# Kernel optimization log

Measured on AMD Instinct MI355X. Metric: run time of the kernel, lower is better.

The kernel has to match this reference:

```python
import jax, jax.numpy as jnp
import numpy as np

CHUNK = 128


def selective_scan(x, A, Bm, Cm, dt, chunk_size):
    # x: [B,L,H,hd], Bm/Cm: [B,L,H,ds], A/dt: [H]. L must be divisible by chunk_size.
    Bb, L, H, hd = x.shape
    ds = Bm.shape[-1]
    cs = chunk_size
    nc = L // cs
    decay = jnp.exp(A * dt)  # [H]
    x_c = x.reshape(Bb, nc, cs, H, hd).transpose(0, 1, 3, 2, 4)   # [B,nc,H,cs,hd]
    B_c = Bm.reshape(Bb, nc, cs, H, ds).transpose(0, 1, 3, 2, 4)  # [B,nc,H,cs,ds]
    C_c = Cm.reshape(Bb, nc, cs, H, ds).transpose(0, 1, 3, 2, 4)
    x_dt = x_c * dt[None, None, :, None, None]
    idx = jnp.arange(cs, dtype=x.dtype)
    diff = idx[:, None] - idx[None, :]
    # causal intra-chunk decay matrix [H,cs,cs]
    L_mat = jnp.where(diff >= 0, decay[:, None, None] ** jnp.maximum(diff, 0.0), 0.0)
    CB = jnp.einsum('bnhid,bnhjd->bnhij', C_c, B_c)          # [B,nc,H,cs,cs]
    y_diag = jnp.einsum('bnhij,bnhjd->bnhid', CB * L_mat[None, None], x_dt)
    rev = jnp.arange(cs - 1, -1, -1, dtype=x.dtype)
    decay_rev = decay[:, None] ** rev[None, :]               # [H,cs]
    B_w = B_c * decay_rev[None, None, :, :, None]
    states = jnp.einsum('bnhjs,bnhjd->bnhsd', B_w, x_dt)     # [B,nc,H,ds,hd]
    cidx = jnp.arange(nc, dtype=x.dtype)
    shift = cidx[:, None] - cidx[None, :] - 1.0
    chunk_decay = decay ** cs
    M = jnp.where(shift >= 0, chunk_decay[:, None, None] ** jnp.maximum(shift, 0.0), 0.0)  # [H,nc,nc]
    h_carry = jnp.einsum('hij,bjhsd->bihsd', M, states)      # [B,nc,H,ds,hd]
    decay_out = decay[:, None] ** (idx[None, :] + 1.0)       # [H,cs]
    y_off = jnp.einsum('bnhis,bnhsd->bnhid', C_c, h_carry) * decay_out[None, None, :, :, None]
    y = (y_diag + y_off).transpose(0, 1, 3, 2, 4).reshape(Bb, L, H, hd)
    return y


def setup_inputs() -> dict:
    key = jax.random.key(0)
    ks = jax.random.split(key, 9)
    B, L, d_model, d_inner, H, ds, K = 2, 4096, 1024, 2048, 16, 128, 4
    s_dm = 1.0 / np.sqrt(d_model)
    s_di = 1.0 / np.sqrt(d_inner)
    x = jax.random.normal(ks[0], (B, L, d_model), jnp.float32)
    x_prenorm = jax.random.normal(ks[1], (B, L, d_model), jnp.float32)
    in_proj_w = jax.random.normal(ks[2], (2 * d_inner, d_model), jnp.float32) * s_dm
    conv_w = jax.random.normal(ks[3], (d_inner, 1, K), jnp.float32) * 0.5
    conv_b = jax.random.normal(ks[4], (d_inner,), jnp.float32) * 0.01
    B_proj_w = jax.random.normal(ks[5], (H * ds, d_model), jnp.float32) * s_dm
    C_proj_w = jax.random.normal(ks[6], (H * ds, d_model), jnp.float32) * s_dm
    dt_init = jax.random.uniform(ks[7], (H,), jnp.float32, 0.001, 0.1)
    dt_bias = dt_init + jnp.log(-jnp.expm1(-dt_init))  # inverse softplus
    A_log = jnp.log(jnp.arange(1, H + 1, dtype=jnp.float32))
    D_param = jnp.ones((H,), jnp.float32)
    out_proj_w = jax.random.normal(ks[8], (d_model, d_inner), jnp.float32) * s_di
    return dict(x=x, x_prenorm=x_prenorm, in_proj_w=in_proj_w, conv_w=conv_w,
                conv_b=conv_b, B_proj_w=B_proj_w, C_proj_w=C_proj_w,
                dt_bias=dt_bias, A_log=A_log, D_param=D_param, out_proj_w=out_proj_w)


def reference(x, x_prenorm, in_proj_w, conv_w, conv_b, B_proj_w, C_proj_w,
              dt_bias, A_log, D_param, out_proj_w):
    Bb, L, d_model = x.shape
    H = A_log.shape[0]
    ds = B_proj_w.shape[0] // H
    vg = x @ in_proj_w.T                        # [B,L,2*d_inner]
    d_inner = vg.shape[-1] // 2
    value, gate = vg[..., :d_inner], vg[..., d_inner:]
    K = conv_w.shape[-1]
    # causal depthwise conv1d (torch pads K-1 both sides then truncates right)
    v = jax.lax.conv_general_dilated(
        value.transpose(0, 2, 1), conv_w, (1,), [(K - 1, 0)],
        feature_group_count=d_inner, dimension_numbers=('NCH', 'OIH', 'NCH'))
    v = v + conv_b[None, :, None]
    value = jax.nn.silu(v.transpose(0, 2, 1))   # [B,L,d_inner]
    Bm = (x_prenorm @ B_proj_w.T).reshape(Bb, L, H, ds)
    Cm = (x_prenorm @ C_proj_w.T).reshape(Bb, L, H, ds)
    dt = jax.nn.softplus(dt_bias)
    A = -jnp.exp(A_log)
    hd = d_inner // H
    vh = value.reshape(Bb, L, H, hd)
    y = selective_scan(vh, A, Bm, Cm, dt, CHUNK)
    y = y + D_param[None, None, :, None] * vh
    y = y.reshape(Bb, L, d_inner) * jax.nn.silu(gate)
    return y @ out_proj_w.T
```

## Files before the change

kernel.cpp:

```cpp
#include <hip/hip_runtime.h>
#include <hip/hip_bf16.h>

#define NB 2
#define LSEQ 4096
#define DM 1024
#define DI 2048
#define NH 16
#define DSZ 128
#define CS 128
#define NCHUNK 32

using bf16 = __hip_bfloat16;
typedef __attribute__((ext_vector_type(8))) short short8;
typedef __attribute__((ext_vector_type(4))) float f32x4;

__device__ __forceinline__ float b2f(unsigned short u) {
    union { unsigned i; float f; } c; c.i = ((unsigned)u) << 16; return c.f;
}
__device__ __forceinline__ bf16 f2bf(float v) { return __float2bfloat16(v); }
__device__ __forceinline__ float bf2f(bf16 v) { return __bfloat162float(v); }

__device__ __forceinline__ float head_dt(const float* dt_bias, int h) {
    return log1pf(expf(dt_bias[h]));
}
__device__ __forceinline__ float head_l2dec(const float* dt_bias, const float* A_log, int h, float* dt_out) {
    float dt = head_dt(dt_bias, h);
    *dt_out = dt;
    return -expf(A_log[h]) * dt * 1.4426950408889634f;
}

__device__ __forceinline__ void storeC(bf16* C, size_t idx, float v) { C[idx] = f2bf(v); }
__device__ __forceinline__ void storeC(float* C, size_t idx, float v) { C[idx] = v; }

__device__ __forceinline__ void gload16(const bf16* g, bf16* l) {
    __builtin_amdgcn_global_load_lds(
        (const __attribute__((address_space(1))) void*)g,
        (__attribute__((address_space(3))) void*)l, 16, 0, 0);
}

__global__ __launch_bounds__(256) void cast_f2b(const float* __restrict__ in,
                                                bf16* __restrict__ out, long n) {
    long i = ((long)blockIdx.x * 256 + threadIdx.x) * 8;
    if (i >= n) return;
    float4 a = *reinterpret_cast<const float4*>(in + i);
    float4 b = *reinterpret_cast<const float4*>(in + i + 4);
    union { bf16 h[8]; short8 v; } o;
    o.h[0] = f2bf(a.x); o.h[1] = f2bf(a.y); o.h[2] = f2bf(a.z); o.h[3] = f2bf(a.w);
    o.h[4] = f2bf(b.x); o.h[5] = f2bf(b.y); o.h[6] = f2bf(b.z); o.h[7] = f2bf(b.w);
    *reinterpret_cast<short8*>(out + i) = o.v;
}

template <int MODE, typename TO>
__global__ __launch_bounds__(256) void gemm_mfma(const bf16* __restrict__ A,
                                                 const bf16* __restrict__ W,
                                                 TO* __restrict__ C0, TO* __restrict__ C1,
                                                 int N, int K) {
    __shared__ bf16 As[2][128 * 32];
    __shared__ bf16 Ws[2][128 * 32];
    const int tid = threadIdx.x;
    const int lane = tid & 63, w = tid >> 6;
    const int wr = w >> 1, wc = w & 1;
    const int bm = blockIdx.y * 128, bn = blockIdx.x * 128;
    const int srow = lane >> 2;
    const int skoff = (((lane & 3) ^ ((lane >> 2) & 3)) * 8);
    const int g0 = w * 2, g1 = w * 2 + 1;
    const int fr = lane & 15;
    const int fk = (((lane >> 4) ^ (lane & 3)) * 8);
    f32x4 acc[4][4] = {};
#define STAGE(buf, kt)                                                                  \
    do {                                                                                \
        gload16(A + (size_t)(bm + g0 * 16 + srow) * K + (kt) + skoff, &As[buf][g0 * 512]); \
        gload16(A + (size_t)(bm + g1 * 16 + srow) * K + (kt) + skoff, &As[buf][g1 * 512]); \
        gload16(W + (size_t)(bn + g0 * 16 + srow) * K + (kt) + skoff, &Ws[buf][g0 * 512]); \
        gload16(W + (size_t)(bn + g1 * 16 + srow) * K + (kt) + skoff, &Ws[buf][g1 * 512]); \
    } while (0)
    STAGE(0, 0);
    __syncthreads();
    const int NT = K / 32;
    int cur = 0;
    for (int t = 0; t < NT; ++t) {
        if (t + 1 < NT) STAGE(cur ^ 1, (t + 1) * 32);
        short8 af[4], bfr[4];
#pragma unroll
        for (int mi = 0; mi < 4; ++mi)
            af[mi] = *reinterpret_cast<const short8*>(&As[cur][(wr * 64 + mi * 16 + fr) * 32 + fk]);
#pragma unroll
        for (int ni = 0; ni < 4; ++ni)
            bfr[ni] = *reinterpret_cast<const short8*>(&Ws[cur][(wc * 64 + ni * 16 + fr) * 32 + fk]);
#pragma unroll
        for (int mi = 0; mi < 4; ++mi)
#pragma unroll
            for (int ni = 0; ni < 4; ++ni)
                acc[mi][ni] = __builtin_amdgcn_mfma_f32_16x16x32_bf16(af[mi], bfr[ni], acc[mi][ni], 0, 0, 0);
        __syncthreads();
        cur ^= 1;
    }
#undef STAGE
    const int orow0 = (lane >> 4) * 4;
    const int ocol = lane & 15;
#pragma unroll
    for (int mi = 0; mi < 4; ++mi)
#pragma unroll
        for (int ni = 0; ni < 4; ++ni) {
            int col = bn + wc * 64 + ni * 16 + ocol;
#pragma unroll
            for (int r = 0; r < 4; ++r) {
                int row = bm + wr * 64 + mi * 16 + orow0 + r;
                float v = acc[mi][ni][r];
                if (MODE == 1) {
                    if (col < DI) storeC(C0, (size_t)row * DI + col, v);
                    else          storeC(C1, (size_t)row * DI + (col - DI), v);
                } else {
                    storeC(C0, (size_t)row * N + col, v);
                }
            }
        }
}

__global__ __launch_bounds__(256) void conv_xdt(const bf16* __restrict__ vpre,
                                                const float* __restrict__ cw,
                                                const float* __restrict__ cb,
                                                const float* __restrict__ dt_bias,
                                                bf16* __restrict__ XDT) {
    __shared__ bf16 Ts[131][136];
    __shared__ bf16 T2[128][136];
    __shared__ float wks[128][4];
    __shared__ float cbs[128];
    const int tid = threadIdx.x;
    const int bid = blockIdx.x;
    const int h = bid & 15, g = bid >> 4;
    const int n31 = g & 31;
    const float dt = head_dt(dt_bias, h);
    if (tid < 128) {
        float4 w4 = *reinterpret_cast<const float4*>(cw + (h * 128 + tid) * 4);
        wks[tid][0] = w4.x; wks[tid][1] = w4.y; wks[tid][2] = w4.z; wks[tid][3] = w4.w;
        cbs[tid] = cb[h * 128 + tid];
    }
    {
        const int lr = tid >> 4, c8 = (tid & 15) * 8;
        for (int i0 = 0; i0 < 144; i0 += 16) {
            int i = i0 + lr;
            if (i < 131) {
                short8 v = {0, 0, 0, 0, 0, 0, 0, 0};
                if (!(n31 == 0 && i < 3))
                    v = *reinterpret_cast<const short8*>(vpre + (size_t)(g * 128 - 3 + i) * 2048 + h * 128 + c8);
                *reinterpret_cast<short8*>(&Ts[i][c8]) = v;
            }
        }
    }
    __syncthreads();
    {
        const int jr = tid >> 4, d8 = (tid & 15) * 8;
        for (int j0 = 0; j0 < 128; j0 += 16) {
            int j = j0 + jr;
            union { bf16 hh[8]; short8 v; } o;
#pragma unroll
            for (int e = 0; e < 8; ++e) {
                int d = d8 + e;
                float s = cbs[d];
#pragma unroll
                for (int k = 0; k < 4; ++k) s += wks[d][k] * bf2f(Ts[j + k][d]);
                float sil = s / (1.f + expf(-s));
                o.hh[e] = f2bf(sil * dt);
            }
            *reinterpret_cast<short8*>(&T2[j][d8]) = o.v;
        }
    }
    __syncthreads();
    {
        const size_t ob = (size_t)bid * 16384;
        const int d = tid & 127;
        for (int jg = (tid >> 7); jg < 16; jg += 2) {
            int j0 = jg * 8;
            union { bf16 hh[8]; short8 v; } o;
#pragma unroll
            for (int e = 0; e < 8; ++e) o.hh[e] = T2[j0 + e][d];
            *reinterpret_cast<short8*>(XDT + ob + (size_t)d * 128 + j0) = o.v;
        }
    }
}

__global__ __launch_bounds__(256) void transpose_bt(const bf16* __restrict__ in, bf16* __restrict__ outp,
                                                    const float* __restrict__ dt_bias,
                                                    const float* __restrict__ A_log) {
    __shared__ bf16 Ts[128][136];
    __shared__ float dpow[128];
    const int tid = threadIdx.x;
    const int bid = blockIdx.x;
    const int h = bid & 15, bn = bid >> 4;
    float dt; float l2d = head_l2dec(dt_bias, A_log, h, &dt);
    if (tid < 128) dpow[tid] = exp2f((float)(127 - tid) * l2d);
    const size_t base = (size_t)bn * CS * 2048 + (size_t)h * 128;
    {
        const int jr = tid >> 4, c8 = (tid & 15) * 8;
        for (int j0 = 0; j0 < 128; j0 += 16)
            *reinterpret_cast<short8*>(&Ts[j0 + jr][c8]) =
                *reinterpret_cast<const short8*>(in + base + (size_t)(j0 + jr) * 2048 + c8);
    }
    __syncthreads();
    const size_t ob = (size_t)bid * 16384;
    const int d = tid & 127;
    for (int jg = (tid >> 7); jg < 16; jg += 2) {
        int j0 = jg * 8;
        union { bf16 h8[8]; short8 v; } o;
#pragma unroll
        for (int e = 0; e < 8; ++e) o.h8[e] = f2bf(bf2f(Ts[j0 + e][d]) * dpow[j0 + e]);
        *reinterpret_cast<short8*>(outp + ob + (size_t)d * 128 + j0) = o.v;
    }
}

__global__ __launch_bounds__(256) void chunk_statesT(const bf16* __restrict__ XDT,
                                                     const bf16* BTg,
                                                     bf16* STT) {
    __shared__ bf16 XTs[128][72];
    __shared__ bf16 BTs[128][72];
    const int tid = threadIdx.x;
    const size_t ob = (size_t)blockIdx.x * 16384;
    const int lane = tid & 63, w = tid >> 6;
    const int fr = lane & 15, fk = (lane >> 4) * 8;
    f32x4 acc[2][8] = {};
    for (int j0 = 0; j0 < 128; j0 += 64) {
        for (int rr = 0; rr < 128; rr += 32) {
            int row = rr + (tid >> 3);
            int col = (tid & 7) * 8;
            *reinterpret_cast<short8*>(&XTs[row][col]) =
                *reinterpret_cast<const short8*>(XDT + ob + (size_t)row * 128 + j0 + col);
            *reinterpret_cast<short8*>(&BTs[row][col]) =
                *reinterpret_cast<const short8*>(BTg + ob + (size_t)row * 128 + j0 + col);
        }
        __syncthreads();
        __builtin_amdgcn_s_setprio(1);
#pragma unroll
        for (int ks = 0; ks < 2; ++ks) {
            short8 a[2], bfr[8];
#pragma unroll
            for (int mi = 0; mi < 2; ++mi)
                a[mi] = *reinterpret_cast<const short8*>(&XTs[w * 32 + mi * 16 + fr][ks * 32 + fk]);
#pragma unroll
            for (int ni = 0; ni < 8; ++ni)
                bfr[ni] = *reinterpret_cast<const short8*>(&BTs[ni * 16 + fr][ks * 32 + fk]);
#pragma unroll
            for (int mi = 0; mi < 2; ++mi)
#pragma unroll
                for (int ni = 0; ni < 8; ++ni)
                    acc[mi][ni] = __builtin_amdgcn_mfma_f32_16x16x32_bf16(a[mi], bfr[ni], acc[mi][ni], 0, 0, 0);
        }
        __builtin_amdgcn_s_setprio(0);
        __syncthreads();
    }
    const int orow0 = (lane >> 4) * 4, ocol = lane & 15;
#pragma unroll
    for (int mi = 0; mi < 2; ++mi)
#pragma unroll
        for (int ni = 0; ni < 8; ++ni) {
            int s = ni * 16 + ocol;
#pragma unroll
            for (int r = 0; r < 4; ++r) {
                int d = w * 32 + mi * 16 + orow0 + r;
                STT[ob + (size_t)d * 128 + s] = f2bf(acc[mi][ni][r]);
            }
        }
}

__global__ __launch_bounds__(256) void scan_kernel(bf16* __restrict__ ST,
                                                   const float* __restrict__ dt_bias,
                                                   const float* __restrict__ A_log) {
    const int q = blockIdx.x & 7;
    const int h = (blockIdx.x >> 3) & 15;
    const int b = blockIdx.x >> 7;
    float dt; float l2d = head_l2dec(dt_bias, A_log, h, &dt);
    float cd = exp2f(128.f * l2d);
    const int tid = threadIdx.x;
    float r[8] = {};
    for (int n = 0; n < NCHUNK; ++n) {
        size_t base = ((size_t)((b * NCHUNK + n) * NH + h)) * 16384 + (size_t)q * 2048;
#pragma unroll
        for (int e = 0; e < 8; ++e) {
            size_t idx = base + e * 256 + tid;
            float v = bf2f(ST[idx]);
            ST[idx] = f2bf(r[e]);
            r[e] = cd * r[e] + v;
        }
    }
}

__global__ __launch_bounds__(256) void chunk_cbl_y(const bf16* __restrict__ Bm, const bf16* __restrict__ Cm,
                                                   const bf16* __restrict__ STT, const bf16* __restrict__ XDT,
                                                   const float* __restrict__ dt_bias,
                                                   const float* __restrict__ A_log,
                                                   const float* __restrict__ D_param,
                                                   bf16* __restrict__ gateY) {
    __shared__ char smem[53248];
    bf16 (*T1)[72]  = reinterpret_cast<bf16(*)[72]>(smem);
    bf16 (*Ps)[136] = reinterpret_cast<bf16(*)[136]>(smem + 18432);
    bf16 (*Bst)[72] = reinterpret_cast<bf16(*)[72]>(smem + 18432);
    const int tid = threadIdx.x;
    const int bid = blockIdx.x;
    const int h = bid & 15, g = bid >> 4;
    float dt; float l2d = head_l2dec(dt_bias, A_log, h, &dt);
    const size_t base = (size_t)g * CS * 2048 + (size_t)h * 128;
    const size_t ob = (size_t)bid * 16384;
    const int lane = tid & 63, w = tid >> 6;
    const int fr = lane & 15, fk = (lane >> 4) * 8;
    const int orow0 = (lane >> 4) * 4, ocol = lane & 15;
    const int strow = tid >> 3, stcol = (tid & 7) * 8;
    f32x4 pacc[2][8] = {};
    for (int s0 = 0; s0 < 128; s0 += 64) {
        for (int rr = 0; rr < 128; rr += 32) {
            int row = rr + strow;
            *reinterpret_cast<short8*>(&T1[row][stcol]) =
                *reinterpret_cast<const short8*>(Cm + base + (size_t)row * 2048 + s0 + stcol);
            *reinterpret_cast<short8*>(&Bst[row][stcol]) =
                *reinterpret_cast<const short8*>(Bm + base + (size_t)row * 2048 + s0 + stcol);
        }
        __syncthreads();
        __builtin_amdgcn_s_setprio(1);
#pragma unroll
        for (int ks = 0; ks < 2; ++ks) {
            short8 a[2], bfr[8];
#pragma unroll
            for (int mi = 0; mi < 2; ++mi)
                a[mi] = *reinterpret_cast<const short8*>(&T1[w * 32 + mi * 16 + fr][ks * 32 + fk]);
#pragma unroll
            for (int ni = 0; ni < 8; ++ni)
                bfr[ni] = *reinterpret_cast<const short8*>(&Bst[ni * 16 + fr][ks * 32 + fk]);
#pragma unroll
            for (int mi = 0; mi < 2; ++mi)
#pragma unroll
                for (int ni = 0; ni < 8; ++ni)
                    pacc[mi][ni] = __builtin_amdgcn_mfma_f32_16x16x32_bf16(a[mi], bfr[ni], pacc[mi][ni], 0, 0, 0);
        }
        __builtin_amdgcn_s_setprio(0);
        __syncthreads();
    }
#pragma unroll
    for (int mi = 0; mi < 2; ++mi)
#pragma unroll
        for (int ni = 0; ni < 8; ++ni) {
            int j = ni * 16 + ocol;
#pragma unroll
            for (int r = 0; r < 4; ++r) {
                int i = w * 32 + mi * 16 + orow0 + r;
                float v = (i >= j) ? pacc[mi][ni][r] * exp2f((float)(i - j) * l2d) : 0.f;
                Ps[i][j] = f2bf(v);
            }
        }
    f32x4 acc[2][8] = {};
    for (int hk = 0; hk < 2; ++hk) {
        for (int rr = 0; rr < 128; rr += 32) {
            int row = rr + strow;
            *reinterpret_cast<short8*>(&T1[row][stcol]) =
                *reinterpret_cast<const short8*>(STT + ob + (size_t)row * 128 + hk * 64 + stcol);
        }
        __syncthreads();
        __builtin_amdgcn_s_setprio(1);
#pragma unroll
        for (int ks = 0; ks < 2; ++ks) {
            short8 a[2], bfr[8];
#pragma unroll
            for (int mi = 0; mi < 2; ++mi)
                a[mi] = *reinterpret_cast<const short8*>(Cm + base + (size_t)(w * 32 + mi * 16 + fr) * 2048 + hk * 64 + ks * 32 + fk);
#pragma unroll
            for (int ni = 0; ni < 8; ++ni)
                bfr[ni] = *reinterpret_cast<const short8*>(&T1[ni * 16 + fr][ks * 32 + fk]);
#pragma unroll
            for (int mi = 0; mi < 2; ++mi)
#pragma unroll
                for (int ni = 0; ni < 8; ++ni)
                    acc[mi][ni] = __builtin_amdgcn_mfma_f32_16x16x32_bf16(a[mi], bfr[ni], acc[mi][ni], 0, 0, 0);
        }
        __builtin_amdgcn_s_setprio(0);
        __syncthreads();
    }
#pragma unroll
    for (int mi = 0; mi < 2; ++mi)
#pragma unroll
        for (int r = 0; r < 4; ++r) {
            int i = w * 32 + mi * 16 + orow0 + r;
            float sc = exp2f((float)(i + 1) * l2d);
#pragma unroll
            for (int ni = 0; ni < 8; ++ni) acc[mi][ni][r] *= sc;
        }
    for (int j0 = 0; j0 < 128; j0 += 64) {
        for (int rr = 0; rr < 128; rr += 32) {
            int row = rr + strow;
            *reinterpret_cast<short8*>(&T1[row][stcol]) =
                *reinterpret_cast<const short8*>(XDT + ob + (size_t)row * 128 + j0 + stcol);
        }
        __syncthreads();
        __builtin_amdgcn_s_setprio(1);
#pragma unroll
        for (int ks = 0; ks < 2; ++ks) {
            short8 a[2], bfr[8];
#pragma unroll
            for (int mi = 0; mi < 2; ++mi)
                a[mi] = *reinterpret_cast<const short8*>(&Ps[w * 32 + mi * 16 + fr][j0 + ks * 32 + fk]);
#pragma unroll
            for (int ni = 0; ni < 8; ++ni)
                bfr[ni] = *reinterpret_cast<const short8*>(&T1[ni * 16 + fr][ks * 32 + fk]);
#pragma unroll
            for (int mi = 0; mi < 2; ++mi)
#pragma unroll
                for (int ni = 0; ni < 8; ++ni)
                    acc[mi][ni] = __builtin_amdgcn_mfma_f32_16x16x32_bf16(a[mi], bfr[ni], acc[mi][ni], 0, 0, 0);
        }
        __builtin_amdgcn_s_setprio(0);
        __syncthreads();
    }
    const float Dv = D_param[h];
    const float inv_dt = 1.f / dt;
#pragma unroll
    for (int mi = 0; mi < 2; ++mi)
#pragma unroll
        for (int ni = 0; ni < 8; ++ni) {
            int d = ni * 16 + ocol;
#pragma unroll
            for (int r = 0; r < 4; ++r) {
                int i = w * 32 + mi * 16 + orow0 + r;
                size_t idx = base + (size_t)i * 2048 + d;
                float v = bf2f(XDT[ob + (size_t)d * 128 + i]) * inv_dt;
                float yv = acc[mi][ni][r] + Dv * v;
                float gq = bf2f(gateY[idx]);
                gateY[idx] = f2bf(yv * gq / (1.f + expf(-gq)));
            }
        }
}

extern "C" void kernel_launch(void* const* d_in, const int* in_sizes, int n_in,
                              void* d_out, int out_size, void* d_ws, size_t ws_size,
                              hipStream_t stream) {
    (void)out_size;
    static const int exp_sizes[11] = {
        NB * LSEQ * DM, NB * LSEQ * DM, 2 * DI * DM, DI * 4, DI,
        NH * DSZ * DM, NH * DSZ * DM, NH, NH, NH, DM * DI
    };
    if (n_in != 11) return;
    for (int i = 0; i < 11; ++i) if (in_sizes[i] != exp_sizes[i]) return;

    const float* x         = (const float*)d_in[0];
    const float* x_prenorm = (const float*)d_in[1];
    const float* in_proj_w = (const float*)d_in[2];
    const float* conv_w    = (const float*)d_in[3];
    const float* conv_b    = (const float*)d_in[4];
    const float* B_proj_w  = (const float*)d_in[5];
    const float* C_proj_w  = (const float*)d_in[6];
    const float* dt_bias   = (const float*)d_in[7];
    const float* A_log     = (const float*)d_in[8];
    const float* D_param   = (const float*)d_in[9];
    const float* out_proj_w= (const float*)d_in[10];
    float* out = (float*)d_out;

    const size_t NE = (size_t)NB * LSEQ * DI;
    const size_t SLOT = NE * 2;
    if (ws_size < 5 * SLOT) return;
    char* ws = (char*)d_ws;
    bf16* S0 = (bf16*)(ws);
    bf16* S1 = (bf16*)(ws + SLOT);
    bf16* S2 = (bf16*)(ws + 2 * SLOT);
    bf16* S3 = (bf16*)(ws + 3 * SLOT);
    bf16* S4 = (bf16*)(ws + 4 * SLOT);

    bf16* xb   = (bf16*)d_out;
    bf16* wBCb = (bf16*)((char*)d_out + 16777216);

    const int M = NB * LSEQ;
    const int NC = NB * NCHUNK * NH;
    dim3 blk(256);

    cast_f2b<<<dim3(4096), blk, 0, stream>>>(x, xb, (long)NB * LSEQ * DM);
    cast_f2b<<<dim3(2048), blk, 0, stream>>>(in_proj_w, S3, (long)2 * DI * DM);
    gemm_mfma<1, bf16><<<dim3(2 * DI / 128, M / 128), blk, 0, stream>>>(xb, S3, S0, S1, 2 * DI, DM);
    conv_xdt<<<dim3(NC), blk, 0, stream>>>(S0, conv_w, conv_b, dt_bias, S2);
    cast_f2b<<<dim3(4096), blk, 0, stream>>>(x_prenorm, xb, (long)NB * LSEQ * DM);
    cast_f2b<<<dim3(1024), blk, 0, stream>>>(B_proj_w, wBCb, (long)NH * DSZ * DM);
    cast_f2b<<<dim3(1024), blk, 0, stream>>>(C_proj_w, wBCb + (size_t)NH * DSZ * DM, (long)NH * DSZ * DM);
    gemm_mfma<1, bf16><<<dim3(2 * DI / 128, M / 128), blk, 0, stream>>>(xb, wBCb, S3, S4, 2 * DI, DM);
    transpose_bt<<<dim3(NC), blk, 0, stream>>>(S3, S0, dt_bias, A_log);
    chunk_statesT<<<dim3(NC), blk, 0, stream>>>(S2, S0, S0);
    scan_kernel<<<dim3(NB * NH * 8), blk, 0, stream>>>(S0, dt_bias, A_log);
    chunk_cbl_y<<<dim3(NC), blk, 0, stream>>>(S3, S4, S0, S2, dt_bias, A_log, D_param, S1);
    cast_f2b<<<dim3(1024), blk, 0, stream>>>(out_proj_w, S3, (long)DM * DI);
    gemm_mfma<2, float><<<dim3(DM / 128, M / 128), blk, 0, stream>>>(S1, S3, out, nullptr, DM, DI);
}
```

Baseline: 385.7 us.

## Fuse B transpose and decay scaling into BC projection GEMM epilogue; merge casts

The B/C projection GEMM gains a mode that, for B-column tiles, stages the tile transposed in shared memory, applies the per-position decay powers and writes the decay-weighted transposed B layout directly. This removes the separate transpose_bt kernel, which re-read B from global memory. The three fp32-to-bf16 casts for x_prenorm and the B/C weights are also merged into one launch. In exchange the GEMM's shared memory grows to hold the transpose buffer and half of its blocks run an extra epilogue.

```diff
diff --git a/kernel.cpp b/kernel.cpp
--- a/kernel.cpp
+++ b/kernel.cpp
@@ -50,13 +50,35 @@
     *reinterpret_cast<short8*>(out + i) = o.v;
 }
 
+__global__ __launch_bounds__(256) void cast3_f2b(const float* __restrict__ a, bf16* __restrict__ da, long na,
+                                                 const float* __restrict__ b, bf16* __restrict__ db, long nb,
+                                                 const float* __restrict__ c, bf16* __restrict__ dc, long nc) {
+    long i = ((long)blockIdx.x * 256 + threadIdx.x) * 8;
+    const float* src; bf16* dst; long off;
+    if (i < na)            { src = a; dst = da; off = i; }
+    else if (i < na + nb)  { src = b; dst = db; off = i - na; }
+    else if (i < na + nb + nc) { src = c; dst = dc; off = i - na - nb; }
+    else return;
+    float4 x = *reinterpret_cast<const float4*>(src + off);
+    float4 y = *reinterpret_cast<const float4*>(src + off + 4);
+    union { bf16 h[8]; short8 v; } o;
+    o.h[0] = f2bf(x.x); o.h[1] = f2bf(x.y); o.h[2] = f2bf(x.z); o.h[3] = f2bf(x.w);
+    o.h[4] = f2bf(y.x); o.h[5] = f2bf(y.y); o.h[6] = f2bf(y.z); o.h[7] = f2bf(y.w);
+    *reinterpret_cast<short8*>(dst + off) = o.v;
+}
+
 template <int MODE, typename TO>
 __global__ __launch_bounds__(256) void gemm_mfma(const bf16* __restrict__ A,
                                                  const bf16* __restrict__ W,
                                                  TO* __restrict__ C0, TO* __restrict__ C1,
+                                                 bf16* __restrict__ C2,
+                                                 const float* dt_bias, const float* A_log,
                                                  int N, int K) {
-    __shared__ bf16 As[2][128 * 32];
-    __shared__ bf16 Ws[2][128 * 32];
+    __shared__ char smem[35328];
+    bf16* Asb = reinterpret_cast<bf16*>(smem);
+    bf16* Wsb = reinterpret_cast<bf16*>(smem + 16384);
+    bf16 (*TP)[136] = reinterpret_cast<bf16(*)[136]>(smem);
+    float* dpw = reinterpret_cast<float*>(smem + 34816);
     const int tid = threadIdx.x;
     const int lane = tid & 63, w = tid >> 6;
     const int wr = w >> 1, wc = w & 1;
@@ -66,13 +88,18 @@
     const int g0 = w * 2, g1 = w * 2 + 1;
     const int fr = lane & 15;
     const int fk = (((lane >> 4) ^ (lane & 3)) * 8);
+    if (MODE == 3 && bn < DI && tid < 128) {
+        float dtq;
+        float l2d = head_l2dec(dt_bias, A_log, blockIdx.x & 15, &dtq);
+        dpw[tid] = exp2f((float)(127 - tid) * l2d);
+    }
     f32x4 acc[4][4] = {};
-#define STAGE(buf, kt)                                                                  \
-    do {                                                                                \
-        gload16(A + (size_t)(bm + g0 * 16 + srow) * K + (kt) + skoff, &As[buf][g0 * 512]); \
-        gload16(A + (size_t)(bm + g1 * 16 + srow) * K + (kt) + skoff, &As[buf][g1 * 512]); \
-        gload16(W + (size_t)(bn + g0 * 16 + srow) * K + (kt) + skoff, &Ws[buf][g0 * 512]); \
-        gload16(W + (size_t)(bn + g1 * 16 + srow) * K + (kt) + skoff, &Ws[buf][g1 * 512]); \
+#define STAGE(buf, kt)                                                                        \
+    do {                                                                                      \
+        gload16(A + (size_t)(bm + g0 * 16 + srow) * K + (kt) + skoff, Asb + (buf) * 4096 + g0 * 512); \
+        gload16(A + (size_t)(bm + g1 * 16 + srow) * K + (kt) + skoff, Asb + (buf) * 4096 + g1 * 512); \
+        gload16(W + (size_t)(bn + g0 * 16 + srow) * K + (kt) + skoff, Wsb + (buf) * 4096 + g0 * 512); \
+        gload16(W + (size_t)(bn + g1 * 16 + srow) * K + (kt) + skoff, Wsb + (buf) * 4096 + g1 * 512); \
     } while (0)
     STAGE(0, 0);
     __syncthreads();
@@ -83,10 +110,10 @@
         short8 af[4], bfr[4];
 #pragma unroll
         for (int mi = 0; mi < 4; ++mi)
-            af[mi] = *reinterpret_cast<const short8*>(&As[cur][(wr * 64 + mi * 16 + fr) * 32 + fk]);
+            af[mi] = *reinterpret_cast<const short8*>(Asb + cur * 4096 + (wr * 64 + mi * 16 + fr) * 32 + fk);
 #pragma unroll
         for (int ni = 0; ni < 4; ++ni)
-            bfr[ni] = *reinterpret_cast<const short8*>(&Ws[cur][(wc * 64 + ni * 16 + fr) * 32 + fk]);
+            bfr[ni] = *reinterpret_cast<const short8*>(Wsb + cur * 4096 + (wc * 64 + ni * 16 + fr) * 32 + fk);
 #pragma unroll
         for (int mi = 0; mi < 4; ++mi)
 #pragma unroll
@@ -107,7 +134,7 @@
             for (int r = 0; r < 4; ++r) {
                 int row = bm + wr * 64 + mi * 16 + orow0 + r;
                 float v = acc[mi][ni][r];
-                if (MODE == 1) {
+                if (MODE == 1 || MODE == 3) {
                     if (col < DI) storeC(C0, (size_t)row * DI + col, v);
                     else          storeC(C1, (size_t)row * DI + (col - DI), v);
                 } else {
@@ -115,6 +142,33 @@
                 }
             }
         }
+    if (MODE == 3 && bn < DI) {
+        __syncthreads();
+#pragma unroll
+        for (int mi = 0; mi < 4; ++mi) {
+            int j0l = wr * 64 + mi * 16 + orow0;
+#pragma unroll
+            for (int ni = 0; ni < 4; ++ni) {
+                int sl = wc * 64 + ni * 16 + ocol;
+                bf16 tmp[4];
+#pragma unroll
+                for (int r = 0; r < 4; ++r) tmp[r] = f2bf(acc[mi][ni][r]);
+                *reinterpret_cast<uint2*>(&TP[sl][j0l]) = *reinterpret_cast<const uint2*>(tmp);
+            }
+        }
+        __syncthreads();
+        const size_t btb = ((size_t)blockIdx.y * 16 + (blockIdx.x & 15)) * 16384;
+        const int s = tid >> 1;
+        const int jh = (tid & 1) * 64;
+#pragma unroll
+        for (int gq = 0; gq < 8; ++gq) {
+            int j = jh + gq * 8;
+            union { bf16 hh[8]; short8 v; } o;
+#pragma unroll
+            for (int e = 0; e < 8; ++e) o.hh[e] = f2bf(bf2f(TP[s][j + e]) * dpw[j + e]);
+            *reinterpret_cast<short8*>(C2 + btb + (size_t)s * 128 + j) = o.v;
+        }
+    }
 }
 
 __global__ __launch_bounds__(256) void conv_xdt(const bf16* __restrict__ vpre,
@@ -177,35 +231,6 @@
             for (int e = 0; e < 8; ++e) o.hh[e] = T2[j0 + e][d];
             *reinterpret_cast<short8*>(XDT + ob + (size_t)d * 128 + j0) = o.v;
         }
-    }
-}
-
-__global__ __launch_bounds__(256) void transpose_bt(const bf16* __restrict__ in, bf16* __restrict__ outp,
-                                                    const float* __restrict__ dt_bias,
-                                                    const float* __restrict__ A_log) {
-    __shared__ bf16 Ts[128][136];
-    __shared__ float dpow[128];
-    const int tid = threadIdx.x;
-    const int bid = blockIdx.x;
-    const int h = bid & 15, bn = bid >> 4;
-    float dt; float l2d = head_l2dec(dt_bias, A_log, h, &dt);
-    if (tid < 128) dpow[tid] = exp2f((float)(127 - tid) * l2d);
-    const size_t base = (size_t)bn * CS * 2048 + (size_t)h * 128;
-    {
-        const int jr = tid >> 4, c8 = (tid & 15) * 8;
-        for (int j0 = 0; j0 < 128; j0 += 16)
-            *reinterpret_cast<short8*>(&Ts[j0 + jr][c8]) =
-                *reinterpret_cast<const short8*>(in + base + (size_t)(j0 + jr) * 2048 + c8);
-    }
-    __syncthreads();
-    const size_t ob = (size_t)bid * 16384;
-    const int d = tid & 127;
-    for (int jg = (tid >> 7); jg < 16; jg += 2) {
-        int j0 = jg * 8;
-        union { bf16 h8[8]; short8 v; } o;
-#pragma unroll
-        for (int e = 0; e < 8; ++e) o.h8[e] = f2bf(bf2f(Ts[j0 + e][d]) * dpow[j0 + e]);
-        *reinterpret_cast<short8*>(outp + ob + (size_t)d * 128 + j0) = o.v;
     }
 }
 
@@ -466,19 +491,23 @@
     const int M = NB * LSEQ;
     const int NC = NB * NCHUNK * NH;
     dim3 blk(256);
-
-    cast_f2b<<<dim3(4096), blk, 0, stream>>>(x, xb, (long)NB * LSEQ * DM);
+    const long nXP = (long)NB * LSEQ * DM;
+    const long nW  = (long)NH * DSZ * DM;
+
+    cast_f2b<<<dim3(4096), blk, 0, stream>>>(x, xb, nXP);
     cast_f2b<<<dim3(2048), blk, 0, stream>>>(in_proj_w, S3, (long)2 * DI * DM);
-    gemm_mfma<1, bf16><<<dim3(2 * DI / 128, M / 128), blk, 0, stream>>>(xb, S3, S0, S1, 2 * DI, DM);
+    gemm_mfma<1, bf16><<<dim3(2 * DI / 128, M / 128), blk, 0, stream>>>(
+        xb, S3, S0, S1, nullptr, nullptr, nullptr, 2 * DI, DM);
     conv_xdt<<<dim3(NC), blk, 0, stream>>>(S0, conv_w, conv_b, dt_bias, S2);
-    cast_f2b<<<dim3(4096), blk, 0, stream>>>(x_prenorm, xb, (long)NB * LSEQ * DM);
-    cast_f2b<<<dim3(1024), blk, 0, stream>>>(B_proj_w, wBCb, (long)NH * DSZ * DM);
-    cast_f2b<<<dim3(1024), blk, 0, stream>>>(C_proj_w, wBCb + (size_t)NH * DSZ * DM, (long)NH * DSZ * DM);
-    gemm_mfma<1, bf16><<<dim3(2 * DI / 128, M / 128), blk, 0, stream>>>(xb, wBCb, S3, S4, 2 * DI, DM);
-    transpose_bt<<<dim3(NC), blk, 0, stream>>>(S3, S0, dt_bias, A_log);
+    cast3_f2b<<<dim3(6144), blk, 0, stream>>>(x_prenorm, xb, nXP,
+                                              B_proj_w, wBCb, nW,
+                                              C_proj_w, wBCb + nW, nW);
+    gemm_mfma<3, bf16><<<dim3(2 * DI / 128, M / 128), blk, 0, stream>>>(
+        xb, wBCb, S3, S4, S0, dt_bias, A_log, 2 * DI, DM);
     chunk_statesT<<<dim3(NC), blk, 0, stream>>>(S2, S0, S0);
     scan_kernel<<<dim3(NB * NH * 8), blk, 0, stream>>>(S0, dt_bias, A_log);
     chunk_cbl_y<<<dim3(NC), blk, 0, stream>>>(S3, S4, S0, S2, dt_bias, A_log, D_param, S1);
     cast_f2b<<<dim3(1024), blk, 0, stream>>>(out_proj_w, S3, (long)DM * DI);
-    gemm_mfma<2, float><<<dim3(DM / 128, M / 128), blk, 0, stream>>>(S1, S3, out, nullptr, DM, DI);
-}
+    gemm_mfma<2, float><<<dim3(DM / 128, M / 128), blk, 0, stream>>>(
+        S1, S3, out, nullptr, nullptr, nullptr, nullptr, DM, DI);
+}
```

Result: faster. 373.1 us (median of 2 runs) (-3.3%).
